# Performance work log

Hardware: AMD Instinct MI355X
Metric: run time of the kernel (lower is better)

Reference implementation:

```python
import jax, jax.numpy as jnp
import numpy as np

B, T, C = 2048, 64, 384  # batch, seq (== block_size), n_embd
HEAD = 64


def setup_inputs() -> dict:
    key = jax.random.key(0)
    k1, k2, k3, k4 = jax.random.split(key, 4)
    x = jax.random.normal(k1, (B, T, C), dtype=jnp.float32)
    Wq = jax.random.normal(k2, (C, HEAD), dtype=jnp.float32) * (C ** -0.5)
    Wk = jax.random.normal(k3, (C, HEAD), dtype=jnp.float32) * (C ** -0.5)
    Wv = jax.random.normal(k4, (C, HEAD), dtype=jnp.float32) * (C ** -0.5)
    return {"x": x, "Wq": Wq, "Wk": Wk, "Wv": Wv}


def reference(x, Wq, Wk, Wv):
    Bx, Tx, Cx = x.shape
    q = jnp.einsum('btc,ch->bth', x, Wq)
    k = jnp.einsum('btc,ch->bth', x, Wk)
    v = jnp.einsum('btc,ch->bth', x, Wv)
    # NOTE: original code scales by n_embd**-0.5 (C), not head_size**-0.5
    wei = jnp.einsum('bth,bsh->bts', q, k) * (Cx ** -0.5)
    causal = jnp.tril(jnp.ones((Tx, Tx), dtype=bool))  # tril[:T,:T]
    wei = jnp.where(causal, wei, -jnp.inf)
    wei = jax.nn.softmax(wei, axis=-1)
    # dropout is identity in eval mode
    out = jnp.einsum('bts,bsh->bth', wei, v)
    return out
```

## Files before the change

kernel.cpp:

```cpp
#include <hip/hip_runtime.h>
#include <stdint.h>

typedef _Float16 f16;
typedef _Float16 f16x8 __attribute__((ext_vector_type(8)));
typedef _Float16 f16x4 __attribute__((ext_vector_type(4)));
typedef float floatx4 __attribute__((ext_vector_type(4)));
typedef float floatx2 __attribute__((ext_vector_type(2)));

#define TT 64
#define CDIM 384
#define HH 64
#define NK2 6
#define LDP 72
#define OST 66
#define CHUNK2 24576
#define C2H 12288
#define ARENA 4608
#define SCALE 0.05103103630798288f

__global__ void prep_w(const float* __restrict__ Wq,
                       const float* __restrict__ Wk,
                       const float* __restrict__ Wv,
                       f16* __restrict__ wf) {
    int t = blockIdx.x * 256 + threadIdx.x;
    if (t >= 3 * 12 * 4 * 64) return;
    int lane = t & 63;
    int tile = (t >> 6) & 3;
    int p    = (t >> 8) % 3;
    int kk   = t / 768;
    const float* W = (p == 0) ? Wq : ((p == 1) ? Wk : Wv);
    int n  = tile * 16 + (lane & 15);
    int k0 = kk * 32 + (lane >> 4) * 8;
    f16x8 frag;
#pragma unroll
    for (int j = 0; j < 8; ++j) frag[j] = (f16)W[(k0 + j) * HH + n];
    ((f16x8*)wf)[t] = frag;
}

static __device__ __forceinline__ f16x8 cvt8(float4 f0, float4 f1) {
    f16x8 h;
    h[0]=(f16)f0.x; h[1]=(f16)f0.y; h[2]=(f16)f0.z; h[3]=(f16)f0.w;
    h[4]=(f16)f1.x; h[5]=(f16)f1.y; h[6]=(f16)f1.z; h[7]=(f16)f1.w;
    return h;
}

static __device__ __forceinline__ void glds16(const void* g, void* l) {
    __builtin_amdgcn_global_load_lds(
        (const __attribute__((address_space(1))) uint32_t*)g,
        (__attribute__((address_space(3))) uint32_t*)l, 16, 0, 0);
}

__launch_bounds__(512, 4)
__global__ void attn_head(const float* __restrict__ x,
                          const f16* __restrict__ wf,
                          float* __restrict__ out) {
    __shared__ __align__(16) char smem[6 * ARENA * sizeof(f16)];
    f16* wbuf = (f16*)smem;

    const int b0   = blockIdx.x * 2;
    const int tid  = threadIdx.x;
    const int wave = tid >> 6;
    const int lane = tid & 63;
    const int quad = lane >> 4;
    const int cl   = lane & 15;
    const int bb   = wave >> 2;
    const int row0b = (wave & 3) * 16;

    const floatx4 fzero = {0.f, 0.f, 0.f, 0.f};
    floatx4 acc[12];
#pragma unroll
    for (int T = 0; T < 12; ++T) acc[T] = fzero;

    const float* xp = x + ((size_t)blockIdx.x * 128 + wave * 16 + cl) * CDIM + quad * 8;
    const char* wb  = (const char*)wf;

    float4 xa[2][2], xb[2][2];
#pragma unroll
    for (int j = 0; j < 3; ++j)
        glds16(wb + j * 8192 + tid * 16, wbuf + j * 4096 + wave * 512);
    asm volatile("" ::: "memory");
#pragma unroll
    for (int s = 0; s < 2; ++s) {
        xa[0][s] = *(const float4*)(xp + s * 32);
        xb[0][s] = *(const float4*)(xp + s * 32 + 4);
    }
    asm volatile("" ::: "memory");

#pragma unroll
    for (int kk = 0; kk < NK2; ++kk) {
        asm volatile("s_waitcnt vmcnt(4)" ::: "memory");
        __builtin_amdgcn_s_barrier();
        if (kk + 1 < NK2) {
            const int nb = (kk + 1) & 1;
#pragma unroll
            for (int j = 0; j < 3; ++j)
                glds16(wb + (kk + 1) * CHUNK2 + j * 8192 + tid * 16,
                       wbuf + nb * C2H + j * 4096 + wave * 512);
            asm volatile("" ::: "memory");
#pragma unroll
            for (int s = 0; s < 2; ++s) {
                xa[nb][s] = *(const float4*)(xp + (kk + 1) * 64 + s * 32);
                xb[nb][s] = *(const float4*)(xp + (kk + 1) * 64 + s * 32 + 4);
            }
            asm volatile("" ::: "memory");
        }
        const int cur = kk & 1;
        const f16* wc = wbuf + cur * C2H;
        f16x8 xf0 = cvt8(xa[cur][0], xb[cur][0]);
        f16x8 xf1 = cvt8(xa[cur][1], xb[cur][1]);
        __builtin_amdgcn_s_setprio(1);
#pragma unroll
        for (int T = 0; T < 12; ++T) {
            f16x8 bf0 = *(const f16x8*)&wc[(T * 64 + lane) * 8];
            acc[T] = __builtin_amdgcn_mfma_f32_16x16x32_f16(xf0, bf0, acc[T], 0, 0, 0);
        }
#pragma unroll
        for (int T = 0; T < 12; ++T) {
            f16x8 bf1 = *(const f16x8*)&wc[6144 + (T * 64 + lane) * 8];
            acc[T] = __builtin_amdgcn_mfma_f32_16x16x32_f16(xf1, bf1, acc[T], 0, 0, 0);
        }
        __builtin_amdgcn_s_setprio(0);
    }
    __syncthreads();

    f16* qs  = (f16*)smem + bb * 3 * ARENA;
    f16* ksm = qs + ARENA;
    f16* vst = qs + 2 * ARENA;
    f16* ps  = qs;
#pragma unroll
    for (int T = 0; T < 12; ++T) {
        int p = T >> 2;
        int h = (T & 3) * 16 + cl;
        if (p == 2) {
            f16x4 vv;
            vv[0]=(f16)acc[T][0]; vv[1]=(f16)acc[T][1];
            vv[2]=(f16)acc[T][2]; vv[3]=(f16)acc[T][3];
            *(f16x4*)&vst[h * LDP + row0b + quad * 4] = vv;
        } else if (p == 0) {
#pragma unroll
            for (int r = 0; r < 4; ++r)
                qs[(row0b + quad * 4 + r) * LDP + h] = (f16)(acc[T][r] * SCALE);
        } else {
#pragma unroll
            for (int r = 0; r < 4; ++r)
                ksm[(row0b + quad * 4 + r) * LDP + h] = (f16)acc[T][r];
        }
    }
    __syncthreads();

    floatx4 sa[4];
#pragma unroll
    for (int t = 0; t < 4; ++t) sa[t] = fzero;
#pragma unroll
    for (int kv = 0; kv < 2; ++kv) {
        f16x8 aq = *(const f16x8*)&qs[(row0b + cl) * LDP + kv * 32 + quad * 8];
#pragma unroll
        for (int t = 0; t < 4; ++t) {
            f16x8 bk = *(const f16x8*)&ksm[(t * 16 + cl) * LDP + kv * 32 + quad * 8];
            sa[t] = __builtin_amdgcn_mfma_f32_16x16x32_f16(aq, bk, sa[t], 0, 0, 0);
        }
    }

#pragma unroll
    for (int t = 0; t < 4; ++t) {
        int s = t * 16 + cl;
#pragma unroll
        for (int r = 0; r < 4; ++r) {
            int tr = row0b + quad * 4 + r;
            float p = (s <= tr) ? __expf(sa[t][r]) : 0.0f;
            ps[tr * LDP + s] = (f16)p;
        }
    }

    floatx4 oa[4];
    floatx4 den = fzero;
#pragma unroll
    for (int t = 0; t < 4; ++t) oa[t] = fzero;
    f16x8 ones;
#pragma unroll
    for (int j = 0; j < 8; ++j) ones[j] = (f16)1.0f;
#pragma unroll
    for (int kv = 0; kv < 2; ++kv) {
        f16x8 ap = *(const f16x8*)&ps[(row0b + cl) * LDP + kv * 32 + quad * 8];
        den = __builtin_amdgcn_mfma_f32_16x16x32_f16(ap, ones, den, 0, 0, 0);
#pragma unroll
        for (int t = 0; t < 4; ++t) {
            f16x8 bv = *(const f16x8*)&vst[(t * 16 + cl) * LDP + kv * 32 + quad * 8];
            oa[t] = __builtin_amdgcn_mfma_f32_16x16x32_f16(ap, bv, oa[t], 0, 0, 0);
        }
    }
    float rden[4];
#pragma unroll
    for (int r = 0; r < 4; ++r) rden[r] = 1.0f / den[r];
    __syncthreads();

    float* ost = (float*)smem + bb * (TT * OST);
#pragma unroll
    for (int t = 0; t < 4; ++t)
#pragma unroll
        for (int r = 0; r < 4; ++r)
            ost[(row0b + quad * 4 + r) * OST + t * 16 + cl] = oa[t][r] * rden[r];
    __syncthreads();

    const int sb   = tid >> 8;
    const int tid2 = tid & 255;
    const float* osb = (const float*)smem + sb * (TT * OST);
    float* op = out + ((size_t)b0 + sb) * TT * HH;
#pragma unroll
    for (int i = 0; i < 4; ++i) {
        int row = i * 16 + (tid2 >> 4);
        int c4  = (tid2 & 15) * 4;
        floatx2 lo = *(const floatx2*)&osb[row * OST + c4];
        floatx2 hi = *(const floatx2*)&osb[row * OST + c4 + 2];
        float4 v; v.x = lo[0]; v.y = lo[1]; v.z = hi[0]; v.w = hi[1];
        *(float4*)&op[row * HH + c4] = v;
    }
}

extern "C" void kernel_launch(void* const* d_in, const int* in_sizes, int n_in,
                              void* d_out, int out_size, void* d_ws, size_t ws_size,
                              hipStream_t stream) {
    const float* x  = (const float*)d_in[0];
    const float* Wq = (const float*)d_in[1];
    const float* Wk = (const float*)d_in[2];
    const float* Wv = (const float*)d_in[3];
    float* out = (float*)d_out;
    f16* wf = (f16*)d_ws;

    prep_w<<<36, 256, 0, stream>>>(Wq, Wk, Wv, wf);
    attn_head<<<1024, 512, 0, stream>>>(x, wf, out);
}
```

Measured before the change: 295.8 us.

## Switch projection to 32x32x16 MFMA with 256-thread blocks and direct output stores

The QKV projection now uses 32x32x16 MFMA tiles, with each wave covering 32 rows instead of 16. The weight fragments are repacked to match, and the block shrinks to 4 waves. The larger tiles cut shared-memory weight reads per FLOP and the instruction count. The attention phase now runs two 16-row groups per wave, and the output is written directly to global memory rather than staged through shared memory, which removes a barrier and an LDS round trip. The trade-offs are fewer waves per block, more register pressure from floatx16 accumulators, and scattered 4-byte global stores instead of coalesced float4 writes.

```diff
diff --git a/kernel.cpp b/kernel.cpp
--- a/kernel.cpp
+++ b/kernel.cpp
@@ -5,17 +5,16 @@
 typedef _Float16 f16x8 __attribute__((ext_vector_type(8)));
 typedef _Float16 f16x4 __attribute__((ext_vector_type(4)));
 typedef float floatx4 __attribute__((ext_vector_type(4)));
-typedef float floatx2 __attribute__((ext_vector_type(2)));
+typedef float floatx16 __attribute__((ext_vector_type(16)));
 
 #define TT 64
 #define CDIM 384
 #define HH 64
-#define NK2 6
+#define NKK 6
 #define LDP 72
-#define OST 66
-#define CHUNK2 24576
-#define C2H 12288
 #define ARENA 4608
+#define CHUNKB 24576
+#define CHH 12288
 #define SCALE 0.05103103630798288f
 
 __global__ void prep_w(const float* __restrict__ Wq,
@@ -23,14 +22,15 @@
                        const float* __restrict__ Wv,
                        f16* __restrict__ wf) {
     int t = blockIdx.x * 256 + threadIdx.x;
-    if (t >= 3 * 12 * 4 * 64) return;
+    if (t >= 24 * 3 * 2 * 64) return;
     int lane = t & 63;
-    int tile = (t >> 6) & 3;
-    int p    = (t >> 8) % 3;
-    int kk   = t / 768;
+    int t2   = (t >> 6) & 1;
+    int g    = t >> 7;
+    int p    = g % 3;
+    int ks   = g / 3;
     const float* W = (p == 0) ? Wq : ((p == 1) ? Wk : Wv);
-    int n  = tile * 16 + (lane & 15);
-    int k0 = kk * 32 + (lane >> 4) * 8;
+    int n  = t2 * 32 + (lane & 31);
+    int k0 = ks * 16 + (lane >> 5) * 8;
     f16x8 frag;
 #pragma unroll
     for (int j = 0; j < 8; ++j) frag[j] = (f16)W[(k0 + j) * HH + n];
@@ -50,170 +50,169 @@
         (__attribute__((address_space(3))) uint32_t*)l, 16, 0, 0);
 }
 
-__launch_bounds__(512, 4)
+__launch_bounds__(256, 2)
 __global__ void attn_head(const float* __restrict__ x,
                           const f16* __restrict__ wf,
                           float* __restrict__ out) {
     __shared__ __align__(16) char smem[6 * ARENA * sizeof(f16)];
     f16* wbuf = (f16*)smem;
 
-    const int b0   = blockIdx.x * 2;
     const int tid  = threadIdx.x;
     const int wave = tid >> 6;
     const int lane = tid & 63;
+    const int l31  = lane & 31;
+    const int lhi  = lane >> 5;
     const int quad = lane >> 4;
     const int cl   = lane & 15;
-    const int bb   = wave >> 2;
-    const int row0b = (wave & 3) * 16;
-
-    const floatx4 fzero = {0.f, 0.f, 0.f, 0.f};
-    floatx4 acc[12];
-#pragma unroll
-    for (int T = 0; T < 12; ++T) acc[T] = fzero;
-
-    const float* xp = x + ((size_t)blockIdx.x * 128 + wave * 16 + cl) * CDIM + quad * 8;
+
+    const floatx16 az = {0.f,0.f,0.f,0.f,0.f,0.f,0.f,0.f,
+                         0.f,0.f,0.f,0.f,0.f,0.f,0.f,0.f};
+    floatx16 acc[6];
+#pragma unroll
+    for (int T = 0; T < 6; ++T) acc[T] = az;
+
+    const float* xp = x + ((size_t)blockIdx.x * 128 + wave * 32 + l31) * CDIM + lhi * 8;
     const char* wb  = (const char*)wf;
 
-    float4 xa[2][2], xb[2][2];
-#pragma unroll
-    for (int j = 0; j < 3; ++j)
-        glds16(wb + j * 8192 + tid * 16, wbuf + j * 4096 + wave * 512);
+    float4 xa[2][4], xb[2][4];
+#pragma unroll
+    for (int j = 0; j < 6; ++j)
+        glds16(wb + j * 4096 + tid * 16, wbuf + j * 2048 + wave * 512);
     asm volatile("" ::: "memory");
 #pragma unroll
-    for (int s = 0; s < 2; ++s) {
-        xa[0][s] = *(const float4*)(xp + s * 32);
-        xb[0][s] = *(const float4*)(xp + s * 32 + 4);
+    for (int s = 0; s < 4; ++s) {
+        xa[0][s] = *(const float4*)(xp + s * 16);
+        xb[0][s] = *(const float4*)(xp + s * 16 + 4);
     }
     asm volatile("" ::: "memory");
 
 #pragma unroll
-    for (int kk = 0; kk < NK2; ++kk) {
-        asm volatile("s_waitcnt vmcnt(4)" ::: "memory");
+    for (int kk = 0; kk < NKK; ++kk) {
+        asm volatile("s_waitcnt vmcnt(8)" ::: "memory");
         __builtin_amdgcn_s_barrier();
-        if (kk + 1 < NK2) {
+        if (kk + 1 < NKK) {
             const int nb = (kk + 1) & 1;
 #pragma unroll
-            for (int j = 0; j < 3; ++j)
-                glds16(wb + (kk + 1) * CHUNK2 + j * 8192 + tid * 16,
-                       wbuf + nb * C2H + j * 4096 + wave * 512);
+            for (int j = 0; j < 6; ++j)
+                glds16(wb + (kk + 1) * CHUNKB + j * 4096 + tid * 16,
+                       wbuf + nb * CHH + j * 2048 + wave * 512);
             asm volatile("" ::: "memory");
 #pragma unroll
-            for (int s = 0; s < 2; ++s) {
-                xa[nb][s] = *(const float4*)(xp + (kk + 1) * 64 + s * 32);
-                xb[nb][s] = *(const float4*)(xp + (kk + 1) * 64 + s * 32 + 4);
+            for (int s = 0; s < 4; ++s) {
+                xa[nb][s] = *(const float4*)(xp + (kk + 1) * 64 + s * 16);
+                xb[nb][s] = *(const float4*)(xp + (kk + 1) * 64 + s * 16 + 4);
             }
             asm volatile("" ::: "memory");
         }
         const int cur = kk & 1;
-        const f16* wc = wbuf + cur * C2H;
-        f16x8 xf0 = cvt8(xa[cur][0], xb[cur][0]);
-        f16x8 xf1 = cvt8(xa[cur][1], xb[cur][1]);
+        const f16* wc = wbuf + cur * CHH;
         __builtin_amdgcn_s_setprio(1);
 #pragma unroll
-        for (int T = 0; T < 12; ++T) {
-            f16x8 bf0 = *(const f16x8*)&wc[(T * 64 + lane) * 8];
-            acc[T] = __builtin_amdgcn_mfma_f32_16x16x32_f16(xf0, bf0, acc[T], 0, 0, 0);
-        }
-#pragma unroll
-        for (int T = 0; T < 12; ++T) {
-            f16x8 bf1 = *(const f16x8*)&wc[6144 + (T * 64 + lane) * 8];
-            acc[T] = __builtin_amdgcn_mfma_f32_16x16x32_f16(xf1, bf1, acc[T], 0, 0, 0);
+        for (int ks = 0; ks < 4; ++ks) {
+            f16x8 af = cvt8(xa[cur][ks], xb[cur][ks]);
+#pragma unroll
+            for (int T = 0; T < 6; ++T) {
+                f16x8 bf = *(const f16x8*)&wc[((ks * 6 + T) * 64 + lane) * 8];
+                acc[T] = __builtin_amdgcn_mfma_f32_32x32x16_f16(af, bf, acc[T], 0, 0, 0);
+            }
         }
         __builtin_amdgcn_s_setprio(0);
     }
     __syncthreads();
 
+    const int bb  = wave >> 1;
+    const int rb0 = (wave & 1) * 32;
     f16* qs  = (f16*)smem + bb * 3 * ARENA;
     f16* ksm = qs + ARENA;
     f16* vst = qs + 2 * ARENA;
     f16* ps  = qs;
-#pragma unroll
-    for (int T = 0; T < 12; ++T) {
-        int p = T >> 2;
-        int h = (T & 3) * 16 + cl;
+    const int hv = 4 * lhi;
+#pragma unroll
+    for (int T = 0; T < 6; ++T) {
+        const int p = T >> 1;
+        const int h = (T & 1) * 32 + l31;
         if (p == 2) {
-            f16x4 vv;
-            vv[0]=(f16)acc[T][0]; vv[1]=(f16)acc[T][1];
-            vv[2]=(f16)acc[T][2]; vv[3]=(f16)acc[T][3];
-            *(f16x4*)&vst[h * LDP + row0b + quad * 4] = vv;
+#pragma unroll
+            for (int g = 0; g < 4; ++g) {
+                f16x4 vv;
+#pragma unroll
+                for (int i = 0; i < 4; ++i) vv[i] = (f16)acc[T][g * 4 + i];
+                *(f16x4*)&vst[h * LDP + rb0 + g * 8 + hv] = vv;
+            }
         } else if (p == 0) {
 #pragma unroll
+            for (int g = 0; g < 4; ++g)
+#pragma unroll
+                for (int i = 0; i < 4; ++i)
+                    qs[(rb0 + g * 8 + hv + i) * LDP + h] = (f16)(acc[T][g * 4 + i] * SCALE);
+        } else {
+#pragma unroll
+            for (int g = 0; g < 4; ++g)
+#pragma unroll
+                for (int i = 0; i < 4; ++i)
+                    ksm[(rb0 + g * 8 + hv + i) * LDP + h] = (f16)acc[T][g * 4 + i];
+        }
+    }
+    __syncthreads();
+
+    const floatx4 fzero = {0.f, 0.f, 0.f, 0.f};
+    const size_t obase = ((size_t)blockIdx.x * 2 + bb) * (TT * HH);
+    f16x8 ones;
+#pragma unroll
+    for (int j = 0; j < 8; ++j) ones[j] = (f16)1.0f;
+
+#pragma unroll
+    for (int g2 = 0; g2 < 2; ++g2) {
+        const int row0 = rb0 + g2 * 16;
+
+        floatx4 sa[4];
+#pragma unroll
+        for (int t = 0; t < 4; ++t) sa[t] = fzero;
+#pragma unroll
+        for (int kv = 0; kv < 2; ++kv) {
+            f16x8 aq = *(const f16x8*)&qs[(row0 + cl) * LDP + kv * 32 + quad * 8];
+#pragma unroll
+            for (int t = 0; t < 4; ++t) {
+                f16x8 bk = *(const f16x8*)&ksm[(t * 16 + cl) * LDP + kv * 32 + quad * 8];
+                sa[t] = __builtin_amdgcn_mfma_f32_16x16x32_f16(aq, bk, sa[t], 0, 0, 0);
+            }
+        }
+
+#pragma unroll
+        for (int t = 0; t < 4; ++t) {
+            int s = t * 16 + cl;
+#pragma unroll
+            for (int r = 0; r < 4; ++r) {
+                int tr = row0 + quad * 4 + r;
+                float p = (s <= tr) ? __expf(sa[t][r]) : 0.0f;
+                ps[tr * LDP + s] = (f16)p;
+            }
+        }
+
+        floatx4 oa[4];
+        floatx4 den = fzero;
+#pragma unroll
+        for (int t = 0; t < 4; ++t) oa[t] = fzero;
+#pragma unroll
+        for (int kv = 0; kv < 2; ++kv) {
+            f16x8 ap = *(const f16x8*)&ps[(row0 + cl) * LDP + kv * 32 + quad * 8];
+            den = __builtin_amdgcn_mfma_f32_16x16x32_f16(ap, ones, den, 0, 0, 0);
+#pragma unroll
+            for (int t = 0; t < 4; ++t) {
+                f16x8 bv = *(const f16x8*)&vst[(t * 16 + cl) * LDP + kv * 32 + quad * 8];
+                oa[t] = __builtin_amdgcn_mfma_f32_16x16x32_f16(ap, bv, oa[t], 0, 0, 0);
+            }
+        }
+        float rden[4];
+#pragma unroll
+        for (int r = 0; r < 4; ++r) rden[r] = 1.0f / den[r];
+
+        float* op = out + obase;
+#pragma unroll
+        for (int t = 0; t < 4; ++t)
+#pragma unroll
             for (int r = 0; r < 4; ++r)
-                qs[(row0b + quad * 4 + r) * LDP + h] = (f16)(acc[T][r] * SCALE);
-        } else {
-#pragma unroll
-            for (int r = 0; r < 4; ++r)
-                ksm[(row0b + quad * 4 + r) * LDP + h] = (f16)acc[T][r];
-        }
-    }
-    __syncthreads();
-
-    floatx4 sa[4];
-#pragma unroll
-    for (int t = 0; t < 4; ++t) sa[t] = fzero;
-#pragma unroll
-    for (int kv = 0; kv < 2; ++kv) {
-        f16x8 aq = *(const f16x8*)&qs[(row0b + cl) * LDP + kv * 32 + quad * 8];
-#pragma unroll
-        for (int t = 0; t < 4; ++t) {
-            f16x8 bk = *(const f16x8*)&ksm[(t * 16 + cl) * LDP + kv * 32 + quad * 8];
-            sa[t] = __builtin_amdgcn_mfma_f32_16x16x32_f16(aq, bk, sa[t], 0, 0, 0);
-        }
-    }
-
-#pragma unroll
-    for (int t = 0; t < 4; ++t) {
-        int s = t * 16 + cl;
-#pragma unroll
-        for (int r = 0; r < 4; ++r) {
-            int tr = row0b + quad * 4 + r;
-            float p = (s <= tr) ? __expf(sa[t][r]) : 0.0f;
-            ps[tr * LDP + s] = (f16)p;
-        }
-    }
-
-    floatx4 oa[4];
-    floatx4 den = fzero;
-#pragma unroll
-    for (int t = 0; t < 4; ++t) oa[t] = fzero;
-    f16x8 ones;
-#pragma unroll
-    for (int j = 0; j < 8; ++j) ones[j] = (f16)1.0f;
-#pragma unroll
-    for (int kv = 0; kv < 2; ++kv) {
-        f16x8 ap = *(const f16x8*)&ps[(row0b + cl) * LDP + kv * 32 + quad * 8];
-        den = __builtin_amdgcn_mfma_f32_16x16x32_f16(ap, ones, den, 0, 0, 0);
-#pragma unroll
-        for (int t = 0; t < 4; ++t) {
-            f16x8 bv = *(const f16x8*)&vst[(t * 16 + cl) * LDP + kv * 32 + quad * 8];
-            oa[t] = __builtin_amdgcn_mfma_f32_16x16x32_f16(ap, bv, oa[t], 0, 0, 0);
-        }
-    }
-    float rden[4];
-#pragma unroll
-    for (int r = 0; r < 4; ++r) rden[r] = 1.0f / den[r];
-    __syncthreads();
-
-    float* ost = (float*)smem + bb * (TT * OST);
-#pragma unroll
-    for (int t = 0; t < 4; ++t)
-#pragma unroll
-        for (int r = 0; r < 4; ++r)
-            ost[(row0b + quad * 4 + r) * OST + t * 16 + cl] = oa[t][r] * rden[r];
-    __syncthreads();
-
-    const int sb   = tid >> 8;
-    const int tid2 = tid & 255;
-    const float* osb = (const float*)smem + sb * (TT * OST);
-    float* op = out + ((size_t)b0 + sb) * TT * HH;
-#pragma unroll
-    for (int i = 0; i < 4; ++i) {
-        int row = i * 16 + (tid2 >> 4);
-        int c4  = (tid2 & 15) * 4;
-        floatx2 lo = *(const floatx2*)&osb[row * OST + c4];
-        floatx2 hi = *(const floatx2*)&osb[row * OST + c4 + 2];
-        float4 v; v.x = lo[0]; v.y = lo[1]; v.z = hi[0]; v.w = hi[1];
-        *(float4*)&op[row * HH + c4] = v;
+                op[(row0 + quad * 4 + r) * HH + t * 16 + cl] = oa[t][r] * rden[r];
     }
 }
 
@@ -228,5 +227,5 @@
     f16* wf = (f16*)d_ws;
 
     prep_w<<<36, 256, 0, stream>>>(Wq, Wk, Wv, wf);
-    attn_head<<<1024, 512, 0, stream>>>(x, wf, out);
-}
+    attn_head<<<1024, 256, 0, stream>>>(x, wf, out);
+}
```

Result: no change. 299.9 us (+1.4%).
